# Performance work log

Measured on AMD Instinct MI355X. Metric: run time of the kernel, lower is better.

Reference implementation:

```python
import jax, jax.numpy as jnp
import numpy as np

LAYERS = [1024, 2048, 1024]
OPTIONS = 4
BATCH = 2048


def setup_inputs() -> dict:
    key = jax.random.key(0)
    k_x, k_idx, k_w1, k_w2 = jax.random.split(key, 4)
    x = jax.random.normal(k_x, (BATCH, LAYERS[0]), dtype=jnp.float32)
    idx = jax.random.randint(k_idx, (BATCH,), 0, OPTIONS, dtype=jnp.int64)
    # xavier-normal-ish scaled weights per layer: shape [options, in, out]
    std1 = float(np.sqrt(2.0 / (LAYERS[0] * LAYERS[1] + OPTIONS * LAYERS[1])))
    std2 = float(np.sqrt(2.0 / (LAYERS[1] * LAYERS[2] + OPTIONS * LAYERS[2])))
    W1 = jax.random.normal(k_w1, (OPTIONS, LAYERS[0], LAYERS[1]), dtype=jnp.float32) * std1
    b1 = jnp.zeros((OPTIONS, LAYERS[1]), dtype=jnp.float32)
    W2 = jax.random.normal(k_w2, (OPTIONS, LAYERS[1], LAYERS[2]), dtype=jnp.float32) * std2
    b2 = jnp.zeros((OPTIONS, LAYERS[2]), dtype=jnp.float32)
    return {"x": x, "idx": idx, "W1": W1, "b1": b1, "W2": W2, "b2": b2}


def reference(x, idx, W1, b1, W2, b2):
    # Original: torch.bmm(x[:,None,:], W[idx]) + b[zeros_like(idx)]
    # Equivalent math without materializing the [B, in, out] gathered weights:
    # compute all options densely, then select per-sample option with idx.
    # NOTE: bias is ALWAYS option 0 (faithful to the original's zeros_like(idx)).
    def layer(h, W, b):
        h_all = jnp.einsum('bi,oij->boj', h, W)  # [B, O, out]
        h_sel = jnp.take_along_axis(h_all, idx[:, None, None], axis=1)[:, 0, :]  # [B, out]
        return h_sel + b[0][None, :]

    h = layer(x, W1, b1)
    out = layer(h, W2, b2)
    return out
```

## Files before the change

kernel.cpp:

```cpp
#include <hip/hip_runtime.h>
#include <stdint.h>

typedef __bf16 bf16x8 __attribute__((ext_vector_type(8)));
typedef float f32x4 __attribute__((ext_vector_type(4)));
typedef unsigned short u16;
typedef const __attribute__((address_space(1))) void* as1_cvp;
typedef __attribute__((address_space(3))) void* as3_vp;

__device__ __forceinline__ u16 f2bf(float f) {
  union { float f; unsigned u; } v; v.f = f;
  unsigned r = v.u + 0x7fffu + ((v.u >> 16) & 1u);
  return (u16)(r >> 16);
}

__device__ void hist_body(const int* __restrict__ idx, int n,
                          int* __restrict__ starts, int* __restrict__ perm,
                          int* __restrict__ tmap64,
                          int* cnt , int* gmeta ) {
  int (*c4)[256] = (int(*)[256])cnt;
  int* gtot = gmeta;
  int* gstart = gmeta + 4;
  const int t = threadIdx.x;
  const int rpt = (n + 255) >> 8;
  const int base = t * rpt;
  int c[4] = {0, 0, 0, 0};
  for (int j = 0; j < rpt; ++j) {
    const int i = base + j;
    if (i < n) c[idx[i] & 3]++;
  }
  #pragma unroll
  for (int g = 0; g < 4; ++g) c4[g][t] = c[g];
  __syncthreads();
  const int w = t >> 6, l = t & 63;
  {
    const int s0 = c4[w][l * 4 + 0], s1 = c4[w][l * 4 + 1];
    const int s2 = c4[w][l * 4 + 2], s3 = c4[w][l * 4 + 3];
    const int sum = s0 + s1 + s2 + s3;
    int sc = sum;
    #pragma unroll
    for (int d = 1; d < 64; d <<= 1) {
      const int o = __shfl_up(sc, d, 64);
      if (l >= d) sc += o;
    }
    const int ex = sc - sum;
    c4[w][l * 4 + 0] = ex;
    c4[w][l * 4 + 1] = ex + s0;
    c4[w][l * 4 + 2] = ex + s0 + s1;
    c4[w][l * 4 + 3] = ex + s0 + s1 + s2;
    if (l == 63) gtot[w] = sc;
  }
  __syncthreads();
  if (t == 0) {
    int s = 0, nt64 = 0;
    for (int g = 0; g < 4; ++g) {
      gstart[g] = s;
      starts[g] = s;
      const int cg = gtot[g];
      for (int j = 0; j < cg; j += 64) tmap64[nt64++] = (g << 28) | (s + j);
      s += cg;
    }
    starts[4] = s;
    while (nt64 < 40) tmap64[nt64++] = -1;
  }
  __syncthreads();
  int run[4] = {0, 0, 0, 0};
  for (int j = 0; j < rpt; ++j) {
    const int i = base + j;
    if (i < n) {
      const int g = idx[i] & 3;
      perm[gstart[g] + c4[g][t] + run[g]] = i;
      run[g]++;
    }
  }
}

__device__ __forceinline__ void wtrans_body(
    float (*tile)[65], const float* __restrict__ W, u16* __restrict__ WT,
    int K, int N, int tx, int ty, int o) {
  const float* Wo = W + (size_t)o * K * N;
  u16* WTo = WT + (size_t)o * N * K;
  const int k0 = ty * 64, n0 = tx * 64;
  const int rr = threadIdx.x >> 4, cc = threadIdx.x & 15;
  #pragma unroll
  for (int j = 0; j < 4; ++j) {
    const int r = j * 16 + rr;
    const float4 v = *(const float4*)(Wo + (size_t)(k0 + r) * N + n0 + cc * 4);
    tile[r][cc * 4 + 0] = v.x; tile[r][cc * 4 + 1] = v.y;
    tile[r][cc * 4 + 2] = v.z; tile[r][cc * 4 + 3] = v.w;
  }
  __syncthreads();
  #pragma unroll
  for (int j = 0; j < 4; ++j) {
    const int nrow = j * 16 + rr;
    ushort4 u;
    u.x = f2bf(tile[cc * 4 + 0][nrow]);
    u.y = f2bf(tile[cc * 4 + 1][nrow]);
    u.z = f2bf(tile[cc * 4 + 2][nrow]);
    u.w = f2bf(tile[cc * 4 + 3][nrow]);
    *(ushort4*)(WTo + (size_t)(n0 + nrow) * K + k0 + cc * 4) = u;
  }
}

__global__ __launch_bounds__(256) void w1t_hist_kernel(
    const float* __restrict__ W1, u16* __restrict__ W1T,
    const int* __restrict__ idx, int n, int* __restrict__ starts,
    int* __restrict__ perm, int* __restrict__ tmap64) {
  __shared__ float tile[64][65];
  const int bid = blockIdx.x;
  if (bid == 2048) {
    hist_body(idx, n, starts, perm, tmap64,
              (int*)&tile[0][0], (int*)&tile[32][0]);
    return;
  }
  const int xcd = bid & 7, i = bid >> 3;
  const int tx = (xcd << 2) | (i & 3);
  const int ty = (i >> 2) & 15;
  const int o = i >> 6;
  wtrans_body(tile, W1, W1T, 1024, 2048, tx, ty, o);
}

__global__ __launch_bounds__(256) void gather_kernel(
    const float* __restrict__ x, const int* __restrict__ perm,
    u16* __restrict__ Xs) {
  const int p = blockIdx.x;
  const int b = perm[p];
  const float4 v = ((const float4*)(x + (size_t)b * 1024))[threadIdx.x];
  ushort4 u;
  u.x = f2bf(v.x); u.y = f2bf(v.y); u.z = f2bf(v.z); u.w = f2bf(v.w);
  ((ushort4*)(Xs + (size_t)p * 1024))[threadIdx.x] = u;
}

template <int EPI, int TM, int NT_PAD, int KT, int NN, int NTN, int SPLIT>
__device__ __forceinline__ void gemm_body(
    char* smem, int bid,
    const u16* __restrict__ A, const u16* __restrict__ BT,
    const float* __restrict__ bias, const int* __restrict__ starts,
    const int* __restrict__ tmap, float* __restrict__ outP,
    u16* __restrict__ outH) {
  constexpr int MR = TM / 32;
  constexpr int ABUF = TM * 128;
  constexpr int BSTR = ABUF + 16384;

  const int nwg = NT_PAD * NTN * SPLIT;
  const int q = nwg >> 3;
  const int swz = (bid & 7) * q + (bid >> 3);
  const int tile = swz % NT_PAD;
  const int rest = swz / NT_PAD;
  const int n_t = rest % NTN;
  const int s = rest / NTN;

  const int tm = tmap[tile];
  if (tm < 0) return;
  const int o = tm >> 28;
  const int m_start = tm & 0x0FFFFFFF;
  const int g1 = starts[o + 1];
  const int n_start = n_t * 128;
  const int kb0 = s * (KT / SPLIT);
  const u16* Bo = BT + (size_t)o * NN * KT;

  const int tid = threadIdx.x;
  const int w = tid >> 6;
  const int l = tid & 63;
  const int wm = w >> 1, wn = w & 1;
  const int l8 = l & 7, ld8 = l >> 3;

  const int src_unit = l8 ^ (ld8 & 7);

  const u16* pA[MR];
  #pragma unroll
  for (int j = 0; j < MR; ++j) {
    int r = m_start + (j * 4 + w) * 8 + ld8;
    if (r >= g1) r = g1 - 1;
    pA[j] = A + (size_t)r * KT + kb0 + src_unit * 8;
  }
  const u16* pB[4];
  #pragma unroll
  for (int j = 0; j < 4; ++j) {
    const int nr = n_start + (j * 4 + w) * 8 + ld8;
    pB[j] = Bo + (size_t)nr * KT + kb0 + src_unit * 8;
  }

#define STAGE(dst_off)                                                         \
  {                                                                            \
    _Pragma("unroll")                                                          \
    for (int j = 0; j < MR; ++j)                                               \
      __builtin_amdgcn_global_load_lds((as1_cvp)pA[j],                         \
          (as3_vp)(smem + (dst_off) + (j * 4 + w) * 1024), 16, 0, 0);          \
    _Pragma("unroll")                                                          \
    for (int j = 0; j < 4; ++j)                                                \
      __builtin_amdgcn_global_load_lds((as1_cvp)pB[j],                         \
          (as3_vp)(smem + (dst_off) + ABUF + (j * 4 + w) * 1024), 16, 0, 0);   \
    _Pragma("unroll") for (int j = 0; j < MR; ++j) pA[j] += 64;                \
    _Pragma("unroll") for (int j = 0; j < 4; ++j) pB[j] += 64;                 \
  }

  const int lrow = l & 15;
  const int lx = l & 7;
  const int lu = l >> 4;
  int offA[MR][2], offB[4][2];
  #pragma unroll
  for (int a = 0; a < MR; ++a)
    #pragma unroll
    for (int kk = 0; kk < 2; ++kk)
      offA[a][kk] = (wm * (TM / 2) + a * 16 + lrow) * 128 + (((kk * 4 + lu) ^ lx) << 4);
  #pragma unroll
  for (int b = 0; b < 4; ++b)
    #pragma unroll
    for (int kk = 0; kk < 2; ++kk)
      offB[b][kk] = (wn * 64 + b * 16 + lrow) * 128 + (((kk * 4 + lu) ^ lx) << 4);

  f32x4 acc[MR][4] = {};

  const int nK = (KT / SPLIT) >> 6;
  STAGE(0);
  for (int kt = 0; kt < nK; ++kt) {
    const int cur = (kt & 1) * BSTR;
    if (kt + 1 < nK) {
      STAGE(BSTR - cur);
      if constexpr (TM == 128)
        asm volatile("s_waitcnt vmcnt(8)" ::: "memory");
      else
        asm volatile("s_waitcnt vmcnt(6)" ::: "memory");
    } else {
      asm volatile("s_waitcnt vmcnt(0)" ::: "memory");
    }
    __builtin_amdgcn_s_barrier();

    bf16x8 af[MR][2], bfr[4][2];
    #pragma unroll
    for (int a = 0; a < MR; ++a)
      #pragma unroll
      for (int kk = 0; kk < 2; ++kk)
        af[a][kk] = *(const bf16x8*)(smem + cur + offA[a][kk]);
    #pragma unroll
    for (int b = 0; b < 4; ++b)
      #pragma unroll
      for (int kk = 0; kk < 2; ++kk)
        bfr[b][kk] = *(const bf16x8*)(smem + cur + ABUF + offB[b][kk]);
    asm volatile("s_waitcnt lgkmcnt(0)" ::: "memory");
    __builtin_amdgcn_s_barrier();

    __builtin_amdgcn_s_setprio(1);
    #pragma unroll
    for (int kk = 0; kk < 2; ++kk)
      #pragma unroll
      for (int a = 0; a < MR; ++a)
        #pragma unroll
        for (int b = 0; b < 4; ++b)
          acc[a][b] = __builtin_amdgcn_mfma_f32_16x16x32_bf16(af[a][kk], bfr[b][kk], acc[a][b], 0, 0, 0);
    __builtin_amdgcn_s_setprio(0);
  }
#undef STAGE

  const int col_l = l & 15;
  const int row_l = (l >> 4) << 2;
  #pragma unroll
  for (int a = 0; a < MR; ++a) {
    #pragma unroll
    for (int b = 0; b < 4; ++b) {
      const int n = n_start + wn * 64 + b * 16 + col_l;
      float bv = 0.f;
      if (EPI == 0) bv = bias[n];
      #pragma unroll
      for (int r = 0; r < 4; ++r) {
        const int p = m_start + wm * (TM / 2) + a * 16 + row_l + r;
        if (p < g1) {
          if (EPI == 0) {
            outH[(size_t)p * NN + n] = f2bf(acc[a][b][r] + bv);
          } else {
            outP[((size_t)(s * 2048 + p)) * NN + n] = acc[a][b][r];
          }
        }
      }
    }
  }
}

__global__ __launch_bounds__(256, 3) void gemm1_w2t_kernel(
    const u16* __restrict__ Xs, const u16* __restrict__ W1T,
    const float* __restrict__ b1, const int* __restrict__ starts,
    const int* __restrict__ tmap64, u16* __restrict__ Hs,
    const float* __restrict__ W2, u16* __restrict__ W2T) {
  __shared__ char smem[49152];
  const int bid = blockIdx.x;
  if (bid < 640) {
    gemm_body<0, 64, 40, 1024, 2048, 16, 1>(
        smem, bid, Xs, W1T, b1, starts, tmap64, nullptr, Hs);
  } else {
    const int b = bid - 640;
    const int xcd = b & 7, i = b >> 3;
    const int tx = (xcd << 1) | (i & 1);
    const int ty = (i >> 1) & 31;
    const int o = i >> 6;
    wtrans_body((float(*)[65])smem, W2, W2T, 2048, 1024, tx, ty, o);
  }
}

__global__ __launch_bounds__(256, 3) void gemm2s_kernel(
    const u16* __restrict__ Hs, const u16* __restrict__ W2T,
    const int* __restrict__ starts, const int* __restrict__ tmap64,
    float* __restrict__ part) {
  __shared__ char smem[49152];
  gemm_body<1, 64, 40, 2048, 1024, 8, 2>(
      smem, blockIdx.x, Hs, W2T, nullptr, starts, tmap64, part, nullptr);
}

__global__ __launch_bounds__(256) void reduce_kernel(
    const float* __restrict__ part, const float* __restrict__ b2,
    const int* __restrict__ perm, float* __restrict__ out) {
  const int p = blockIdx.x;
  const int t = threadIdx.x;
  const float4 v0 = ((const float4*)(part + (size_t)p * 1024))[t];
  const float4 v1 = ((const float4*)(part + (size_t)(2048 + p) * 1024))[t];
  const float4 bv = ((const float4*)b2)[t];
  float4 r;
  r.x = v0.x + v1.x + bv.x;
  r.y = v0.y + v1.y + bv.y;
  r.z = v0.z + v1.z + bv.z;
  r.w = v0.w + v1.w + bv.w;
  ((float4*)(out + (size_t)perm[p] * 1024))[t] = r;
}

extern "C" void kernel_launch(void* const* d_in, const int* in_sizes, int n_in,
                              void* d_out, int out_size, void* d_ws, size_t ws_size,
                              hipStream_t stream) {
  (void)n_in; (void)out_size; (void)ws_size;
  const float* x   = (const float*)d_in[0];
  const int*   idx = (const int*)d_in[1];
  const float* W1  = (const float*)d_in[2];
  const float* b1  = (const float*)d_in[3];
  const float* W2  = (const float*)d_in[4];
  const float* b2  = (const float*)d_in[5];
  float* out = (float*)d_out;

  const int B = in_sizes[1];

  char* ws = (char*)d_ws;
  u16* W1T     = (u16*)(ws);
  float* part  = (float*)(ws);
  u16* W2T     = (u16*)(ws + 16777216);
  u16* Xs      = (u16*)(ws + 33554432);
  u16* Hs      = (u16*)(ws + 37748736);
  int* perm    = (int*)(ws + 46137344);
  int* starts  = (int*)(ws + 46137344 + 8192);
  int* tmap64  = starts + 128;

  w1t_hist_kernel<<<2049, 256, 0, stream>>>(W1, W1T, idx, B, starts, perm,
                                            tmap64);
  gather_kernel<<<B, 256, 0, stream>>>(x, perm, Xs);
  gemm1_w2t_kernel<<<640 + 2048, 256, 0, stream>>>(
      Xs, W1T, b1, starts, tmap64, Hs, W2, W2T);
  gemm2s_kernel<<<640, 256, 0, stream>>>(Hs, W2T, starts, tmap64, part);
  reduce_kernel<<<B, 256, 0, stream>>>(part, b2, perm, out);
}
```

Measured before the change: 66.41 us.

## Fuse split-K reduction into GEMM2 epilogue via per-tile atomic counter

Removes the separate reduce kernel. Each split-K GEMM2 block writes its partial to the workspace, then bumps a per-output-tile atomic counter. The last-arriving block adds the other partial plus bias and scatters the result to the permuted output row. This saves a kernel launch and a full pass over the partial buffer, at the cost of threadfences, an atomic, and an extra epilogue in half the blocks. The counters are zeroed in the histogram block.

```diff
diff --git a/kernel.cpp b/kernel.cpp
--- a/kernel.cpp
+++ b/kernel.cpp
@@ -104,10 +104,12 @@
 __global__ __launch_bounds__(256) void w1t_hist_kernel(
     const float* __restrict__ W1, u16* __restrict__ W1T,
     const int* __restrict__ idx, int n, int* __restrict__ starts,
-    int* __restrict__ perm, int* __restrict__ tmap64) {
+    int* __restrict__ perm, int* __restrict__ tmap64,
+    int* __restrict__ pcnt) {
   __shared__ float tile[64][65];
   const int bid = blockIdx.x;
   if (bid == 2048) {
+    for (int i = threadIdx.x; i < 320; i += 256) pcnt[i] = 0;
     hist_body(idx, n, starts, perm, tmap64,
               (int*)&tile[0][0], (int*)&tile[32][0]);
     return;
@@ -136,7 +138,8 @@
     const u16* __restrict__ A, const u16* __restrict__ BT,
     const float* __restrict__ bias, const int* __restrict__ starts,
     const int* __restrict__ tmap, float* __restrict__ outP,
-    u16* __restrict__ outH) {
+    u16* __restrict__ outH, const int* __restrict__ perm,
+    float* __restrict__ outF, int* __restrict__ pcnt) {
   constexpr int MR = TM / 32;
   constexpr int ABUF = TM * 128;
   constexpr int BSTR = ABUF + 16384;
@@ -254,21 +257,55 @@
 
   const int col_l = l & 15;
   const int row_l = (l >> 4) << 2;
-  #pragma unroll
-  for (int a = 0; a < MR; ++a) {
-    #pragma unroll
-    for (int b = 0; b < 4; ++b) {
-      const int n = n_start + wn * 64 + b * 16 + col_l;
-      float bv = 0.f;
-      if (EPI == 0) bv = bias[n];
-      #pragma unroll
-      for (int r = 0; r < 4; ++r) {
-        const int p = m_start + wm * (TM / 2) + a * 16 + row_l + r;
-        if (p < g1) {
-          if (EPI == 0) {
-            outH[(size_t)p * NN + n] = f2bf(acc[a][b][r] + bv);
-          } else {
+  if constexpr (EPI == 0) {
+    #pragma unroll
+    for (int a = 0; a < MR; ++a) {
+      #pragma unroll
+      for (int b = 0; b < 4; ++b) {
+        const int n = n_start + wn * 64 + b * 16 + col_l;
+        const float bv = bias[n];
+        #pragma unroll
+        for (int r = 0; r < 4; ++r) {
+          const int p = m_start + wm * (TM / 2) + a * 16 + row_l + r;
+          if (p < g1) outH[(size_t)p * NN + n] = f2bf(acc[a][b][r] + bv);
+        }
+      }
+    }
+  } else {
+    #pragma unroll
+    for (int a = 0; a < MR; ++a) {
+      #pragma unroll
+      for (int b = 0; b < 4; ++b) {
+        const int n = n_start + wn * 64 + b * 16 + col_l;
+        #pragma unroll
+        for (int r = 0; r < 4; ++r) {
+          const int p = m_start + wm * (TM / 2) + a * 16 + row_l + r;
+          if (p < g1)
             outP[((size_t)(s * 2048 + p)) * NN + n] = acc[a][b][r];
+        }
+      }
+    }
+    __threadfence();
+    __syncthreads();
+    __shared__ int s_last;
+    if (tid == 0)
+      s_last = (atomicAdd(&pcnt[tile * NTN + n_t], 1) == 1);
+    __syncthreads();
+    if (s_last) {
+      __threadfence();
+      const size_t so = (size_t)((s ^ 1) * 2048);
+      #pragma unroll
+      for (int a = 0; a < MR; ++a) {
+        #pragma unroll
+        for (int b = 0; b < 4; ++b) {
+          const int n = n_start + wn * 64 + b * 16 + col_l;
+          const float bv = bias[n];
+          #pragma unroll
+          for (int r = 0; r < 4; ++r) {
+            const int p = m_start + wm * (TM / 2) + a * 16 + row_l + r;
+            if (p < g1)
+              outF[(size_t)perm[p] * NN + n] =
+                  (acc[a][b][r] + outP[(so + p) * NN + n]) + bv;
           }
         }
       }
@@ -285,7 +322,8 @@
   const int bid = blockIdx.x;
   if (bid < 640) {
     gemm_body<0, 64, 40, 1024, 2048, 16, 1>(
-        smem, bid, Xs, W1T, b1, starts, tmap64, nullptr, Hs);
+        smem, bid, Xs, W1T, b1, starts, tmap64, nullptr, Hs,
+        nullptr, nullptr, nullptr);
   } else {
     const int b = bid - 640;
     const int xcd = b & 7, i = b >> 3;
@@ -298,27 +336,14 @@
 
 __global__ __launch_bounds__(256, 3) void gemm2s_kernel(
     const u16* __restrict__ Hs, const u16* __restrict__ W2T,
-    const int* __restrict__ starts, const int* __restrict__ tmap64,
-    float* __restrict__ part) {
+    const float* __restrict__ b2, const int* __restrict__ starts,
+    const int* __restrict__ tmap64, float* __restrict__ part,
+    const int* __restrict__ perm, float* __restrict__ out,
+    int* __restrict__ pcnt) {
   __shared__ char smem[49152];
   gemm_body<1, 64, 40, 2048, 1024, 8, 2>(
-      smem, blockIdx.x, Hs, W2T, nullptr, starts, tmap64, part, nullptr);
-}
-
-__global__ __launch_bounds__(256) void reduce_kernel(
-    const float* __restrict__ part, const float* __restrict__ b2,
-    const int* __restrict__ perm, float* __restrict__ out) {
-  const int p = blockIdx.x;
-  const int t = threadIdx.x;
-  const float4 v0 = ((const float4*)(part + (size_t)p * 1024))[t];
-  const float4 v1 = ((const float4*)(part + (size_t)(2048 + p) * 1024))[t];
-  const float4 bv = ((const float4*)b2)[t];
-  float4 r;
-  r.x = v0.x + v1.x + bv.x;
-  r.y = v0.y + v1.y + bv.y;
-  r.z = v0.z + v1.z + bv.z;
-  r.w = v0.w + v1.w + bv.w;
-  ((float4*)(out + (size_t)perm[p] * 1024))[t] = r;
+      smem, blockIdx.x, Hs, W2T, b2, starts, tmap64, part, nullptr,
+      perm, out, pcnt);
 }
 
 extern "C" void kernel_launch(void* const* d_in, const int* in_sizes, int n_in,
@@ -344,12 +369,13 @@
   int* perm    = (int*)(ws + 46137344);
   int* starts  = (int*)(ws + 46137344 + 8192);
   int* tmap64  = starts + 128;
+  int* pcnt    = starts + 512;
 
   w1t_hist_kernel<<<2049, 256, 0, stream>>>(W1, W1T, idx, B, starts, perm,
-                                            tmap64);
+                                            tmap64, pcnt);
   gather_kernel<<<B, 256, 0, stream>>>(x, perm, Xs);
   gemm1_w2t_kernel<<<640 + 2048, 256, 0, stream>>>(
       Xs, W1T, b1, starts, tmap64, Hs, W2, W2T);
-  gemm2s_kernel<<<640, 256, 0, stream>>>(Hs, W2T, starts, tmap64, part);
-  reduce_kernel<<<B, 256, 0, stream>>>(part, b2, perm, out);
-}
+  gemm2s_kernel<<<640, 256, 0, stream>>>(Hs, W2T, b2, starts, tmap64, part,
+                                         perm, out, pcnt);
+}
```

After: 165.1 us. +148.6%, slower.
